# Performance work log

Hardware: AMD Instinct MI355X
Metric: run time of the kernel (lower is better)

The kernel has to match this reference:

```python
import jax, jax.numpy as jnp
import numpy as np

N_NODES = 100000
N_EDGES = 1600000
IN_C = 128
OUT_C = 128


def setup_inputs() -> dict:
    key = jax.random.key(0)
    k1, k2, k3, k4 = jax.random.split(key, 4)
    x = jax.random.normal(k1, (N_NODES, IN_C), dtype=jnp.float32)
    W = jax.random.normal(k2, (IN_C, OUT_C), dtype=jnp.float32) * (1.0 / np.sqrt(IN_C))
    b = jax.random.normal(k3, (OUT_C,), dtype=jnp.float32) * 0.02
    edge_index = jax.random.randint(k4, (2, N_EDGES), 0, N_NODES, dtype=jnp.int32)
    return {"x": x, "W": W, "b": b, "edge_index": edge_index}


def reference(x, W, b, edge_index):
    N = x.shape[0]
    # Symmetrize edges: concat(edge_index, flip(edge_index)) as in adj()
    row = jnp.concatenate([edge_index[0], edge_index[1]])  # [2E]
    col = jnp.concatenate([edge_index[1], edge_index[0]])  # [2E]
    w = jnp.ones(row.shape, dtype=x.dtype)
    # gcn_norm with self loops (fill value 1): deg includes self-loop weight
    deg = jax.ops.segment_sum(w, row, num_segments=N) + 1.0
    dinv = jnp.where(deg > 0, jax.lax.rsqrt(deg), 0.0)  # [N]
    # Dense linear projection (bias=False)
    xw = x @ W  # [N, out]
    # SpMM: y[row] += dinv[row]*dinv[col] * xw[col]  (scatter-add == coalesced adj matmul)
    norm = dinv[row] * dinv[col]  # [2E]
    msgs = norm[:, None] * xw[col]  # [2E, out] -- dominant memory traffic
    y = jax.ops.segment_sum(msgs, row, num_segments=N)
    # Self-loop contribution: weight dinv[i]^2
    y = y + (dinv * dinv)[:, None] * xw
    return y + b
```

## Files before the change

kernel.cpp:

```cpp
#include <hip/hip_runtime.h>
#include <math.h>

constexpr int N = 100000;
constexpr int E = 1600000;
constexpr int C = 128;
constexpr int NPB   = 256;
constexpr int NBUCK = (N + NPB - 1) / NPB;
constexpr int CAP   = 9472;
constexpr int ADJ_STRIDE = CAP + NPB * 7;

typedef __attribute__((ext_vector_type(8))) short bf16x8;
typedef __attribute__((ext_vector_type(4))) float f32x4;

__device__ inline unsigned f2bf(float f) {
    unsigned u = __float_as_uint(f);
    return (u + 0x7fffu + ((u >> 16) & 1u)) >> 16;
}
__device__ inline unsigned pack2(float lo, float hi) {
    return f2bf(lo) | (f2bf(hi) << 16);
}
__device__ inline float bf_lo(unsigned m) { return __uint_as_float(m << 16); }
__device__ inline float bf_hi(unsigned m) { return __uint_as_float(m & 0xffff0000u); }

__global__ __launch_bounds__(256) void k_bin(const int* __restrict__ ei,
                                             int* __restrict__ gcount,
                                             unsigned* __restrict__ staging,
                                             const float* __restrict__ W,
                                             unsigned short* __restrict__ WhiT,
                                             unsigned short* __restrict__ WloT,
                                             unsigned* __restrict__ z16) {
    const int t = threadIdx.x;
    if (blockIdx.x < 64) {
        const int i = blockIdx.x * 256 + t;
        const int k = i >> 7, c = i & 127;
        const float f = W[i];
        const unsigned hb = f2bf(f);
        WhiT[c * 128 + k] = (unsigned short)hb;
        WloT[c * 128 + k] = (unsigned short)f2bf(f - __uint_as_float(hb << 16));
        if (blockIdx.x == 0 && t < 64) z16[(size_t)N * 64 + t] = 0u;
    }
    __shared__ int cnt[NBUCK];
    __shared__ int wbase[NBUCK];
    const long tile = (long)blockIdx.x * 2048;
    for (int i = t; i < NBUCK; i += 256) cnt[i] = 0;
    __syncthreads();
    int b0[8], b1[8], lo0[8], lo1[8];
    unsigned p0[8], p1[8];
    bool val[8];
#pragma unroll
    for (int j = 0; j < 8; ++j) {
        long e = tile + j * 256 + t;
        val[j] = e < E;
        if (val[j]) {
            int u = __builtin_nontemporal_load(ei + e);
            int v = __builtin_nontemporal_load(ei + E + e);
            b0[j] = u >> 8;
            b1[j] = v >> 8;
            p0[j] = ((unsigned)(u & 255) << 17) | (unsigned)v;
            p1[j] = ((unsigned)(v & 255) << 17) | (unsigned)u;
            lo0[j] = atomicAdd(&cnt[b0[j]], 1);
            lo1[j] = atomicAdd(&cnt[b1[j]], 1);
        }
    }
    __syncthreads();
    for (int i = t; i < NBUCK; i += 256) wbase[i] = atomicAdd(&gcount[i], cnt[i]);
    __syncthreads();
#pragma unroll
    for (int j = 0; j < 8; ++j) {
        if (val[j]) {
            staging[(size_t)b0[j] * CAP + wbase[b0[j]] + lo0[j]] = p0[j];
            staging[(size_t)b1[j] * CAP + wbase[b1[j]] + lo1[j]] = p1[j];
        }
    }
}

__global__ __launch_bounds__(512) void k_csr(const unsigned* __restrict__ staging,
                                             const int* __restrict__ gcount,
                                             int* __restrict__ deg,
                                             float* __restrict__ dinv,
                                             int* __restrict__ rowptr,
                                             int* __restrict__ adj) {
    __shared__ int hist[NPB];
    __shared__ int wpart[4];
    const int g = blockIdx.x;
    const int t = threadIdx.x;
    const int lane = t & 63, wid = t >> 6;
    const int cnt = gcount[g];
    int* slice = adj + (size_t)g * ADJ_STRIDE;
    for (int i = t; i < NPB; i += 512) hist[i] = 0;
    __syncthreads();
    const unsigned* base = staging + (size_t)g * CAP;
    for (int i = t; i < cnt; i += 512) atomicAdd(&hist[base[i] >> 17], 1);
    __syncthreads();
    const int d  = (t < NPB) ? hist[t] : 0;
    const int pd = (d + 7) & ~7;
    int v = pd;
#pragma unroll
    for (int off = 1; off < 64; off <<= 1) {
        int n = __shfl_up(v, off);
        if (lane >= off) v += n;
    }
    if (lane == 63 && wid < 4) wpart[wid] = v;
    __syncthreads();
    if (t == 0) {
        int r = 0;
#pragma unroll
        for (int w = 0; w < 4; ++w) { int x = wpart[w]; wpart[w] = r; r += x; }
    }
    __syncthreads();
    const int pstart = v - pd + ((wid < 4) ? wpart[wid] : 0);
    if (t < NPB) {
        const int node = g * NPB + t;
        if (node < N) {
            deg[node]    = d;
            dinv[node]   = rsqrtf((float)d + 1.0f);
            rowptr[node] = g * ADJ_STRIDE + pstart;
        }
        for (int i = d; i < pd; ++i) slice[pstart + i] = N;
    }
    __syncthreads();
    if (t < NPB) hist[t] = pstart;
    __syncthreads();
    for (int i = t; i < cnt; i += 512) {
        const unsigned e = base[i];
        const int pos = atomicAdd(&hist[e >> 17], 1);
        slice[pos] = (int)(e & 0x1ffffu);
    }
}

__global__ __launch_bounds__(256) void k_gemm(const float* __restrict__ x,
                                              const unsigned short* __restrict__ WhiT,
                                              const unsigned short* __restrict__ WloT,
                                              const float* __restrict__ dinv,
                                              unsigned* __restrict__ z16) {
    __shared__ unsigned short xh[64][136];
    __shared__ unsigned short xl[64][136];
    const int t = threadIdx.x;
    const int bid = blockIdx.x;

#pragma unroll
    for (int j = 0; j < 8; ++j) {
        const int f4i = j * 256 + t;
        const int row = f4i >> 5;
        const int k4  = f4i & 31;
        const long gr = (long)bid * 64 + row;
        float4 f = {0.f, 0.f, 0.f, 0.f};
        if (gr < N) f = *(const float4*)(x + gr * C + k4 * 4);
        unsigned hq[4], lq[4];
#pragma unroll
        for (int e = 0; e < 4; ++e) {
            const float fe = (&f.x)[e];
            const unsigned hb = f2bf(fe);
            hq[e] = hb;
            lq[e] = f2bf(fe - __uint_as_float(hb << 16));
        }
        uint2 ph = {hq[0] | (hq[1] << 16), hq[2] | (hq[3] << 16)};
        uint2 pl = {lq[0] | (lq[1] << 16), lq[2] | (lq[3] << 16)};
        *(uint2*)(&xh[row][k4 * 4]) = ph;
        *(uint2*)(&xl[row][k4 * 4]) = pl;
    }
    __syncthreads();

    const int wid = t >> 6, l = t & 63;
    const int nb = wid * 16;
    const int lr = l & 15, lg = l >> 4;

    f32x4 acc[8];
#pragma unroll
    for (int i = 0; i < 8; ++i) acc[i] = (f32x4){0.f, 0.f, 0.f, 0.f};

    const unsigned short* xhp = &xh[nb + lr][lg * 8];
    const unsigned short* xlp = &xl[nb + lr][lg * 8];

#pragma unroll
    for (int kc = 0; kc < 4; ++kc) {
        const bf16x8 bh = *(const bf16x8*)(xhp + kc * 32);
        const bf16x8 bl = *(const bf16x8*)(xlp + kc * 32);
#pragma unroll
        for (int ct = 0; ct < 8; ++ct) {
            const int woff = (ct * 16 + lr) * 128 + kc * 32 + lg * 8;
            const bf16x8 ahi = *(const bf16x8*)(WhiT + woff);
            const bf16x8 alo = *(const bf16x8*)(WloT + woff);
            acc[ct] = __builtin_amdgcn_mfma_f32_16x16x32_bf16(ahi, bh, acc[ct], 0, 0, 0);
            acc[ct] = __builtin_amdgcn_mfma_f32_16x16x32_bf16(ahi, bl, acc[ct], 0, 0, 0);
            acc[ct] = __builtin_amdgcn_mfma_f32_16x16x32_bf16(alo, bh, acc[ct], 0, 0, 0);
        }
    }

    const long node = (long)bid * 64 + nb + lr;
    if (node < N) {
        const float dv = dinv[node];
#pragma unroll
        for (int ct = 0; ct < 8; ++ct) {
            const int ch0 = ct * 16 + lg * 4;
            uint2 pk = {pack2(dv * acc[ct][0], dv * acc[ct][1]),
                        pack2(dv * acc[ct][2], dv * acc[ct][3])};
            *(uint2*)(z16 + node * 64 + ch0 / 2) = pk;
        }
    }
}

__global__ __launch_bounds__(256) void k_gather(const int* __restrict__ rowptr,
                                                const int* __restrict__ deg,
                                                const float* __restrict__ dinv,
                                                const int* __restrict__ adj,
                                                const unsigned* __restrict__ z16,
                                                const float* __restrict__ b,
                                                float* __restrict__ out,
                                                int u0, int u1) {
    const int u = u0 + blockIdx.x * 4 + (threadIdx.x >> 6);
    if (u >= u1) return;
    const int lane = threadIdx.x & 63;
    const int d  = __builtin_amdgcn_readfirstlane(deg[u]);
    const int pd = (d + 7) & ~7;
    const int st = __builtin_amdgcn_readfirstlane(rowptr[u]);
    const float du = dinv[u];

    const unsigned ms = z16[((size_t)(unsigned)u << 6) + lane];
    float ax = bf_lo(ms), ay = bf_hi(ms);

    unsigned q0, q1, q2, q3, q4, q5, q6, q7;
    unsigned r0, r1, r2, r3, r4, r5, r6, r7;

#define ZR(j) z16[((size_t)(unsigned)__builtin_amdgcn_readlane(v, (j)) << 6) + lane]
#define LD8(A, p) A##0 = ZR((p) + 0); A##1 = ZR((p) + 1); A##2 = ZR((p) + 2); \
                  A##3 = ZR((p) + 3); A##4 = ZR((p) + 4); A##5 = ZR((p) + 5); \
                  A##6 = ZR((p) + 6); A##7 = ZR((p) + 7);
#define AC8(A) ax += bf_lo(A##0); ay += bf_hi(A##0); ax += bf_lo(A##1); ay += bf_hi(A##1); \
               ax += bf_lo(A##2); ay += bf_hi(A##2); ax += bf_lo(A##3); ay += bf_hi(A##3); \
               ax += bf_lo(A##4); ay += bf_hi(A##4); ax += bf_lo(A##5); ay += bf_hi(A##5); \
               ax += bf_lo(A##6); ay += bf_hi(A##6); ax += bf_lo(A##7); ay += bf_hi(A##7);

    for (int j0 = 0; j0 < pd; j0 += 64) {
        const int cntc = min(64, pd - j0);
        const int v = adj[st + j0 + lane];
        int p = 8;
        LD8(q, 0);
        for (; p + 16 <= cntc; p += 16) {
            LD8(r, p); AC8(q);
            LD8(q, p + 8); AC8(r);
        }
        if (p < cntc) { LD8(r, p); AC8(q); AC8(r); }
        else          { AC8(q); }
    }
#undef ZR
#undef LD8
#undef AC8

    const float2 bb = *(const float2*)(b + 2 * lane);
    float2 o = {fmaf(du, ax, bb.x), fmaf(du, ay, bb.y)};
    *(float2*)(out + (size_t)u * C + 2 * lane) = o;
}

extern "C" void kernel_launch(void* const* d_in, const int* in_sizes, int n_in,
                              void* d_out, int out_size, void* d_ws, size_t ws_size,
                              hipStream_t stream) {
    const float* x  = (const float*)d_in[0];
    const float* W  = (const float*)d_in[1];
    const float* b  = (const float*)d_in[2];
    const int*   ei = (const int*)d_in[3];
    float* out = (float*)d_out;

    char* p = (char*)d_ws;
    unsigned* z16 = (unsigned*)p;
    unsigned* staging = z16;
    p += (size_t)(N + 1) * 64 * sizeof(unsigned);
    int* adj = (int*)p;             p += ((size_t)NBUCK * ADJ_STRIDE + 64) * sizeof(int);
    int* deg = (int*)p;             p += (size_t)N * sizeof(int);
    float* dinv = (float*)p;        p += (size_t)N * sizeof(float);
    int* rowptr = (int*)p;          p += (size_t)(N + 4) * sizeof(int);
    int* gcount = (int*)p;          p += 512 * sizeof(int);
    unsigned short* WhiT = (unsigned short*)p;  p += (size_t)C * C * sizeof(unsigned short);
    unsigned short* WloT = (unsigned short*)p;

    hipMemsetAsync(gcount, 0, 512 * sizeof(int), stream);
    k_bin<<<(E + 2047) / 2048, 256, 0, stream>>>(ei, gcount, staging, W, WhiT, WloT, z16);
    k_csr<<<NBUCK, 512, 0, stream>>>(staging, gcount, deg, dinv, rowptr, adj);
    k_gemm<<<(N + 63) / 64, 256, 0, stream>>>(x, WhiT, WloT, dinv, z16);
    const int third = (N + 2) / 3;
    for (int s = 0; s < 3; ++s) {
        const int u0 = s * third;
        const int u1 = (u0 + third < N) ? (u0 + third) : N;
        k_gather<<<(u1 - u0 + 3) / 4, 256, 0, stream>>>(rowptr, deg, dinv, adj, z16, b, out, u0, u1);
    }
}
```

Before: 343.0 us.

## Stage W fragments in LDS and loop persistent GEMM blocks over node tiles

k_bin now writes the bf16 hi/lo split of W in a fragment-ordered layout that matches the MFMA A-operand lane pattern. The GEMM kernel runs as a persistent grid of 512 blocks, copies the whole 64KB fragment array into LDS once, then loops over 64-node tiles. Each lane loads its x row directly from global memory and splits it to bf16 in registers, so the LDS staging of x and its barrier are gone. The aim is to stop re-reading W from global or L2 in every tile and to remove per-tile LDS traffic for x. In exchange, the 64KB of LDS per block limits occupancy, and the per-lane x loads are strided by row.

After: 313.3 us. -8.7%, faster.

```diff
diff --git a/kernel.cpp b/kernel.cpp
--- a/kernel.cpp
+++ b/kernel.cpp
@@ -8,6 +8,7 @@
 constexpr int NBUCK = (N + NPB - 1) / NPB;
 constexpr int CAP   = 9472;
 constexpr int ADJ_STRIDE = CAP + NPB * 7;
+constexpr int NT = (N + 63) / 64;
 
 typedef __attribute__((ext_vector_type(8))) short bf16x8;
 typedef __attribute__((ext_vector_type(4))) float f32x4;
@@ -26,17 +27,19 @@
                                              int* __restrict__ gcount,
                                              unsigned* __restrict__ staging,
                                              const float* __restrict__ W,
-                                             unsigned short* __restrict__ WhiT,
-                                             unsigned short* __restrict__ WloT,
+                                             unsigned short* __restrict__ wfrag,
                                              unsigned* __restrict__ z16) {
     const int t = threadIdx.x;
     if (blockIdx.x < 64) {
         const int i = blockIdx.x * 256 + t;
         const int k = i >> 7, c = i & 127;
+        const int ct = c >> 4, lr = c & 15;
+        const int kc = k >> 5, lg = (k >> 3) & 3, e = k & 7;
+        const int idx = ((ct * 4 + kc) * 64 + lg * 16 + lr) * 8 + e;
         const float f = W[i];
         const unsigned hb = f2bf(f);
-        WhiT[c * 128 + k] = (unsigned short)hb;
-        WloT[c * 128 + k] = (unsigned short)f2bf(f - __uint_as_float(hb << 16));
+        wfrag[idx]         = (unsigned short)hb;
+        wfrag[16384 + idx] = (unsigned short)f2bf(f - __uint_as_float(hb << 16));
         if (blockIdx.x == 0 && t < 64) z16[(size_t)N * 64 + t] = 0u;
     }
     __shared__ int cnt[NBUCK];
@@ -129,73 +132,67 @@
 }
 
 __global__ __launch_bounds__(256) void k_gemm(const float* __restrict__ x,
-                                              const unsigned short* __restrict__ WhiT,
-                                              const unsigned short* __restrict__ WloT,
+                                              const unsigned short* __restrict__ wfrag,
                                               const float* __restrict__ dinv,
                                               unsigned* __restrict__ z16) {
-    __shared__ unsigned short xh[64][136];
-    __shared__ unsigned short xl[64][136];
+    __shared__ unsigned short wlds[32768];
     const int t = threadIdx.x;
-    const int bid = blockIdx.x;
-
-#pragma unroll
-    for (int j = 0; j < 8; ++j) {
-        const int f4i = j * 256 + t;
-        const int row = f4i >> 5;
-        const int k4  = f4i & 31;
-        const long gr = (long)bid * 64 + row;
-        float4 f = {0.f, 0.f, 0.f, 0.f};
-        if (gr < N) f = *(const float4*)(x + gr * C + k4 * 4);
-        unsigned hq[4], lq[4];
-#pragma unroll
-        for (int e = 0; e < 4; ++e) {
-            const float fe = (&f.x)[e];
-            const unsigned hb = f2bf(fe);
-            hq[e] = hb;
-            lq[e] = f2bf(fe - __uint_as_float(hb << 16));
-        }
-        uint2 ph = {hq[0] | (hq[1] << 16), hq[2] | (hq[3] << 16)};
-        uint2 pl = {lq[0] | (lq[1] << 16), lq[2] | (lq[3] << 16)};
-        *(uint2*)(&xh[row][k4 * 4]) = ph;
-        *(uint2*)(&xl[row][k4 * 4]) = pl;
+    {
+        const uint4* src = (const uint4*)wfrag;
+        uint4* dst = (uint4*)wlds;
+#pragma unroll
+        for (int j = 0; j < 16; ++j) dst[t + 256 * j] = src[t + 256 * j];
     }
     __syncthreads();
 
     const int wid = t >> 6, l = t & 63;
-    const int nb = wid * 16;
     const int lr = l & 15, lg = l >> 4;
-
-    f32x4 acc[8];
-#pragma unroll
-    for (int i = 0; i < 8; ++i) acc[i] = (f32x4){0.f, 0.f, 0.f, 0.f};
-
-    const unsigned short* xhp = &xh[nb + lr][lg * 8];
-    const unsigned short* xlp = &xl[nb + lr][lg * 8];
-
-#pragma unroll
-    for (int kc = 0; kc < 4; ++kc) {
-        const bf16x8 bh = *(const bf16x8*)(xhp + kc * 32);
-        const bf16x8 bl = *(const bf16x8*)(xlp + kc * 32);
-#pragma unroll
-        for (int ct = 0; ct < 8; ++ct) {
-            const int woff = (ct * 16 + lr) * 128 + kc * 32 + lg * 8;
-            const bf16x8 ahi = *(const bf16x8*)(WhiT + woff);
-            const bf16x8 alo = *(const bf16x8*)(WloT + woff);
-            acc[ct] = __builtin_amdgcn_mfma_f32_16x16x32_bf16(ahi, bh, acc[ct], 0, 0, 0);
-            acc[ct] = __builtin_amdgcn_mfma_f32_16x16x32_bf16(ahi, bl, acc[ct], 0, 0, 0);
-            acc[ct] = __builtin_amdgcn_mfma_f32_16x16x32_bf16(alo, bh, acc[ct], 0, 0, 0);
-        }
-    }
-
-    const long node = (long)bid * 64 + nb + lr;
-    if (node < N) {
-        const float dv = dinv[node];
-#pragma unroll
-        for (int ct = 0; ct < 8; ++ct) {
-            const int ch0 = ct * 16 + lg * 4;
-            uint2 pk = {pack2(dv * acc[ct][0], dv * acc[ct][1]),
-                        pack2(dv * acc[ct][2], dv * acc[ct][3])};
-            *(uint2*)(z16 + node * 64 + ch0 / 2) = pk;
+    const unsigned short* wl_hi = wlds + l * 8;
+    const unsigned short* wl_lo = wlds + 16384 + l * 8;
+
+    for (int tile = blockIdx.x; tile < NT; tile += gridDim.x) {
+        const long node = (long)tile * 64 + wid * 16 + lr;
+        const bool nv = node < N;
+        const float* xr = x + node * C + lg * 8;
+
+        f32x4 acc[8];
+#pragma unroll
+        for (int i = 0; i < 8; ++i) acc[i] = (f32x4){0.f, 0.f, 0.f, 0.f};
+
+#pragma unroll
+        for (int kc = 0; kc < 4; ++kc) {
+            float4 f0 = {0.f, 0.f, 0.f, 0.f}, f1 = {0.f, 0.f, 0.f, 0.f};
+            if (nv) {
+                f0 = *(const float4*)(xr + kc * 32);
+                f1 = *(const float4*)(xr + kc * 32 + 4);
+            }
+            bf16x8 bh, bl;
+#pragma unroll
+            for (int e = 0; e < 8; ++e) {
+                const float fe = (e < 4) ? (&f0.x)[e] : (&f1.x)[e - 4];
+                const unsigned hb = f2bf(fe);
+                bh[e] = (short)hb;
+                bl[e] = (short)f2bf(fe - __uint_as_float(hb << 16));
+            }
+#pragma unroll
+            for (int ct = 0; ct < 8; ++ct) {
+                const int fo = (ct * 4 + kc) * 512;
+                const bf16x8 ahi = *(const bf16x8*)(wl_hi + fo);
+                const bf16x8 alo = *(const bf16x8*)(wl_lo + fo);
+                acc[ct] = __builtin_amdgcn_mfma_f32_16x16x32_bf16(ahi, bh, acc[ct], 0, 0, 0);
+                acc[ct] = __builtin_amdgcn_mfma_f32_16x16x32_bf16(ahi, bl, acc[ct], 0, 0, 0);
+                acc[ct] = __builtin_amdgcn_mfma_f32_16x16x32_bf16(alo, bh, acc[ct], 0, 0, 0);
+            }
+        }
+
+        if (nv) {
+            const float dv = dinv[node];
+#pragma unroll
+            for (int ct = 0; ct < 8; ++ct) {
+                uint2 pk = {pack2(dv * acc[ct][0], dv * acc[ct][1]),
+                            pack2(dv * acc[ct][2], dv * acc[ct][3])};
+                *(uint2*)(z16 + node * 64 + ct * 8 + lg * 2) = pk;
+            }
         }
     }
 }
@@ -270,13 +267,12 @@
     float* dinv = (float*)p;        p += (size_t)N * sizeof(float);
     int* rowptr = (int*)p;          p += (size_t)(N + 4) * sizeof(int);
     int* gcount = (int*)p;          p += 512 * sizeof(int);
-    unsigned short* WhiT = (unsigned short*)p;  p += (size_t)C * C * sizeof(unsigned short);
-    unsigned short* WloT = (unsigned short*)p;
+    unsigned short* wfrag = (unsigned short*)p;
 
     hipMemsetAsync(gcount, 0, 512 * sizeof(int), stream);
-    k_bin<<<(E + 2047) / 2048, 256, 0, stream>>>(ei, gcount, staging, W, WhiT, WloT, z16);
+    k_bin<<<(E + 2047) / 2048, 256, 0, stream>>>(ei, gcount, staging, W, wfrag, z16);
     k_csr<<<NBUCK, 512, 0, stream>>>(staging, gcount, deg, dinv, rowptr, adj);
-    k_gemm<<<(N + 63) / 64, 256, 0, stream>>>(x, WhiT, WloT, dinv, z16);
+    k_gemm<<<512, 256, 0, stream>>>(x, wfrag, dinv, z16);
     const int third = (N + 2) / 3;
     for (int s = 0; s < 3; ++s) {
         const int u0 = s * third;
```
